# Performance work log

Measured on AMD Instinct MI355X. Metric: run time of the kernel, lower is better.

## Reference

```python
import jax, jax.numpy as jnp
import numpy as np

DIM, HEADS, DIM_HEAD = 1024, 16, 64
DIM_INNER = HEADS * DIM_HEAD  # 1024
SCALE = DIM_HEAD ** -0.5


def _rope(t):
    # t: [b, h, n, d]; interleaved-pair RoPE (lucidrains rotary-embedding-torch default)
    d = t.shape[-1]
    n = t.shape[-2]
    inv_freq = 1.0 / (10000.0 ** (jnp.arange(0, d, 2, dtype=jnp.float32) / d))
    angles = jnp.arange(n, dtype=jnp.float32)[:, None] * inv_freq[None, :]  # [n, d/2]
    cos, sin = jnp.cos(angles), jnp.sin(angles)
    t1, t2 = t[..., 0::2], t[..., 1::2]
    r1 = t1 * cos - t2 * sin
    r2 = t1 * sin + t2 * cos
    return jnp.stack([r1, r2], axis=-1).reshape(t.shape)


def setup_inputs() -> dict:
    key = jax.random.key(0)
    ks = jax.random.split(key, 8)
    b, n = 2, 2048
    inp = {
        "x": jax.random.normal(ks[0], (b, n, DIM), dtype=jnp.float32),
        "value_residual": jax.random.normal(ks[1], (b, HEADS, n, DIM_HEAD), dtype=jnp.float32),
        "gamma": jnp.ones((DIM,), dtype=jnp.float32),
        "w_qkv": jax.random.normal(ks[2], (DIM, 3 * DIM_INNER), dtype=jnp.float32) * (DIM ** -0.5),
        "w_mix": jax.random.normal(ks[3], (DIM, HEADS), dtype=jnp.float32) * (DIM ** -0.5),
        "b_mix": jnp.zeros((HEADS,), dtype=jnp.float32),
        "w_gates": jax.random.normal(ks[4], (DIM, HEADS), dtype=jnp.float32) * (DIM ** -0.5),
        "b_gates": jnp.zeros((HEADS,), dtype=jnp.float32),
        "w_out": jax.random.normal(ks[5], (DIM_INNER, DIM), dtype=jnp.float32) * (DIM_INNER ** -0.5),
    }
    return inp


def reference(x, value_residual, gamma, w_qkv, w_mix, b_mix, w_gates, b_gates, w_out):
    b, n, _ = x.shape
    # RMSNorm (lucidrains style: F.normalize * sqrt(dim) * gamma)
    norm = jnp.sqrt(jnp.sum(x * x, axis=-1, keepdims=True))
    xn = x / jnp.maximum(norm, 1e-12) * (DIM ** 0.5) * gamma

    qkv = xn @ w_qkv  # [b, n, 3*h*d]
    qkv = qkv.reshape(b, n, 3, HEADS, DIM_HEAD)
    q, k, v = [jnp.transpose(qkv[:, :, i], (0, 2, 1, 3)) for i in range(3)]  # [b,h,n,d]
    original_values = v

    # learned value-residual lerp
    mix = jax.nn.sigmoid(xn @ w_mix + b_mix)            # [b, n, h]
    mix = jnp.transpose(mix, (0, 2, 1))[..., None]       # [b, h, n, 1]
    v = v * (1.0 - mix) + value_residual * mix

    # rotary on q, k
    q = _rope(q)
    k = _rope(k)

    scores = jnp.einsum("bhid,bhjd->bhij", q, k) * SCALE
    attn = jax.nn.softmax(scores, axis=-1)
    out = jnp.einsum("bhij,bhjd->bhid", attn, v)         # [b, h, n, d]

    gates = jax.nn.sigmoid(xn @ w_gates + b_gates)       # [b, n, h]
    out = out * jnp.transpose(gates, (0, 2, 1))[..., None]

    out = jnp.transpose(out, (0, 2, 1, 3)).reshape(b, n, DIM_INNER)
    return out @ w_out, original_values
```

## Files before the change

### kernel.cpp

```cpp
#include <hip/hip_runtime.h>
#include <hip/hip_bf16.h>
#include <math.h>

#define DIMSZ 1024
#define HEADS 16
#define DHEAD 64
#define NSEQ  2048
#define BATCH 2
#define ROWS  (BATCH*NSEQ)
#define SCALE 0.125f
#define LOG2E 1.4426950408889634f

typedef __attribute__((ext_vector_type(8))) short short8;
typedef __attribute__((ext_vector_type(4))) float floatx4;

#define MFMA16(a,b,c) __builtin_amdgcn_mfma_f32_16x16x32_bf16(a,b,c,0,0,0)

__device__ __forceinline__ void gl2lds16(const void* g, void* l) {
    __builtin_amdgcn_global_load_lds(
        (const __attribute__((address_space(1))) unsigned int*)g,
        (__attribute__((address_space(3))) unsigned int*)l, 16, 0, 0);
}

__device__ __forceinline__ unsigned short bf16r(float a) {
    unsigned u = __float_as_uint(a);
    u += 0x7fff + ((u >> 16) & 1);
    return (unsigned short)(u >> 16);
}
__device__ __forceinline__ unsigned pack_bf16(float a, float b) {
    unsigned ua = __float_as_uint(a), ub = __float_as_uint(b);
    ua += 0x7fff + ((ua >> 16) & 1);
    ub += 0x7fff + ((ub >> 16) & 1);
    return (ua >> 16) | (ub & 0xffff0000u);
}
__device__ __forceinline__ float2 bf2f(unsigned u) {
    float2 r;
    r.x = __uint_as_float(u << 16);
    r.y = __uint_as_float(u & 0xffff0000u);
    return r;
}
__device__ __forceinline__ float fexp2(float x) {
#if __has_builtin(__builtin_amdgcn_exp2f)
    return __builtin_amdgcn_exp2f(x);
#else
    return exp2f(x);
#endif
}
__device__ __forceinline__ float fsin_rev(float x) {
#if __has_builtin(__builtin_amdgcn_sinf)
    return __builtin_amdgcn_sinf(x);
#else
    return __sinf(x * 6.28318530717958647692f);
#endif
}
__device__ __forceinline__ float fcos_rev(float x) {
#if __has_builtin(__builtin_amdgcn_cosf)
    return __builtin_amdgcn_cosf(x);
#else
    return __cosf(x * 6.28318530717958647692f);
#endif
}

__global__ __launch_bounds__(256) void transpose_all_kernel(
    const float* __restrict__ w_qkv, const float* __restrict__ w_out,
    const float* __restrict__ w_mix, const float* __restrict__ w_gates,
    unsigned short* __restrict__ wqkvT, unsigned short* __restrict__ woutT,
    unsigned short* __restrict__ wmgT)
{
    __shared__ float t[32][33];
    const int tx = threadIdx.x & 31, tyy = threadIdx.x >> 5;
    const int bx = blockIdx.x;
    const int k0 = blockIdx.y * 32;
    if (bx < 128) {
        const float* src;
        unsigned short* dst;
        int N, n0;
        if (bx < 96) { src = w_qkv; dst = wqkvT; N = 3*DIMSZ; n0 = bx*32; }
        else         { src = w_out; dst = woutT; N = DIMSZ;   n0 = (bx-96)*32; }
        #pragma unroll
        for (int i = 0; i < 4; i++)
            t[tyy*4 + i][tx] = src[(size_t)(k0 + tyy*4 + i)*N + n0 + tx];
        __syncthreads();
        #pragma unroll
        for (int i = 0; i < 4; i++)
            dst[(size_t)(n0 + tyy*4 + i)*DIMSZ + k0 + tx] = bf16r(t[tx][tyy*4 + i]);
    } else {
        #pragma unroll
        for (int i = 0; i < 4; i++) {
            const int kk = k0 + tyy*4 + i;
            t[tyy*4 + i][tx] = (tx < 16) ? w_mix[kk*16 + tx]
                                         : w_gates[kk*16 + (tx - 16)];
        }
        __syncthreads();
        #pragma unroll
        for (int i = 0; i < 4; i++)
            wmgT[(size_t)(tyy*4 + i)*DIMSZ + k0 + tx] = bf16r(t[tx][tyy*4 + i]);
    }
}

__global__ __launch_bounds__(256) void rmsnorm_kernel(
    const float* __restrict__ x, const float* __restrict__ gamma,
    unsigned short* __restrict__ xnb)
{
    const int row = blockIdx.x;
    const int tid = threadIdx.x;
    __shared__ float wred[4];

    const float4 xv = ((const float4*)(x + (size_t)row * DIMSZ))[tid];
    float ss = xv.x*xv.x + xv.y*xv.y + xv.z*xv.z + xv.w*xv.w;
    #pragma unroll
    for (int off = 1; off < 64; off <<= 1) ss += __shfl_xor(ss, off);
    if ((tid & 63) == 0) wred[tid >> 6] = ss;
    __syncthreads();
    const float total = wred[0] + wred[1] + wred[2] + wred[3];
    const float inv = 32.0f / fmaxf(sqrtf(total), 1e-12f);
    const float4 gv = ((const float4*)gamma)[tid];
    uint2 pk;
    pk.x = pack_bf16(xv.x * inv * gv.x, xv.y * inv * gv.y);
    pk.y = pack_bf16(xv.z * inv * gv.z, xv.w * inv * gv.w);
    ((uint2*)(xnb + (size_t)row * DIMSZ))[tid] = pk;
}

__global__ __launch_bounds__(256) void mix_gates_mfma(
    const unsigned short* __restrict__ A, const unsigned short* __restrict__ WG,
    const float* __restrict__ b_mix, const float* __restrict__ b_gates,
    float* __restrict__ mixo, float* __restrict__ gateso)
{
    __shared__ short As[128*32];
    __shared__ short Bs[32*32];
    const int tid = threadIdx.x;
    const int wv = tid >> 6, lane = tid & 63;
    const int g = lane >> 4, c = lane & 15;
    const int bm = blockIdx.x * 128;

    floatx4 acc[2][2];
    #pragma unroll
    for (int mt = 0; mt < 2; mt++)
        #pragma unroll
        for (int nt = 0; nt < 2; nt++) acc[mt][nt] = (floatx4){0.f,0.f,0.f,0.f};

    for (int k0 = 0; k0 < DIMSZ; k0 += 32) {
        __syncthreads();
        #pragma unroll
        for (int r = 0; r < 2; r++) {
            const int ch = tid + 256*r;
            const int row = ch >> 2, cc = ch & 3;
            gl2lds16(A + (size_t)(bm + row)*DIMSZ + k0 + cc*8, (void*)(As + ch*8));
        }
        if (tid < 128)
            gl2lds16(WG + (size_t)(tid >> 2)*DIMSZ + k0 + (tid & 3)*8, (void*)(Bs + tid*8));
        __syncthreads();
        short8 af[2], bf[2];
        #pragma unroll
        for (int mt = 0; mt < 2; mt++) af[mt] = *(const short8*)(As + (wv*32 + mt*16 + c)*32 + g*8);
        #pragma unroll
        for (int nt = 0; nt < 2; nt++) bf[nt] = *(const short8*)(Bs + (nt*16 + c)*32 + g*8);
        #pragma unroll
        for (int mt = 0; mt < 2; mt++)
            #pragma unroll
            for (int nt = 0; nt < 2; nt++)
                acc[mt][nt] = MFMA16(af[mt], bf[nt], acc[mt][nt]);
    }
    const float bm_c = b_mix[c], bg_c = b_gates[c];
    #pragma unroll
    for (int mt = 0; mt < 2; mt++)
        #pragma unroll
        for (int r2 = 0; r2 < 4; r2++) {
            const int row = bm + wv*32 + mt*16 + g*4 + r2;
            const float lm = acc[mt][0][r2] + bm_c;
            const float lg = acc[mt][1][r2] + bg_c;
            mixo[(size_t)row*HEADS + c]   = 1.0f / (1.0f + fexp2(-lm * LOG2E));
            gateso[(size_t)row*HEADS + c] = 1.0f / (1.0f + fexp2(-lg * LOG2E));
        }
}

__global__ __launch_bounds__(256) void gemm_qkv_mfma(
    const unsigned short* __restrict__ A, const unsigned short* __restrict__ BT,
    unsigned short* __restrict__ qb, unsigned short* __restrict__ kb,
    float* __restrict__ vb)
{
    __shared__ short As[128*32];
    __shared__ short Bs[128*32];
    const int tid = threadIdx.x;
    const int wv = tid >> 6, lane = tid & 63;
    const int g = lane >> 4, c = lane & 15;
    const int wm = wv >> 1, wn = wv & 1;
    const int bm = blockIdx.y * 128, bn = blockIdx.x * 128;

    floatx4 acc[4][4];
    #pragma unroll
    for (int mt = 0; mt < 4; mt++)
        #pragma unroll
        for (int nt = 0; nt < 4; nt++) acc[mt][nt] = (floatx4){0.f,0.f,0.f,0.f};

    for (int k0 = 0; k0 < DIMSZ; k0 += 32) {
        __syncthreads();
        #pragma unroll
        for (int r = 0; r < 2; r++) {
            const int ch = tid + 256*r;
            const int row = ch >> 2, cc = ch & 3;
            gl2lds16(A  + (size_t)(bm + row)*DIMSZ + k0 + cc*8, (void*)(As + ch*8));
            gl2lds16(BT + (size_t)(bn + row)*DIMSZ + k0 + cc*8, (void*)(Bs + ch*8));
        }
        __syncthreads();
        short8 af[4], bf[4];
        #pragma unroll
        for (int mt = 0; mt < 4; mt++) af[mt] = *(const short8*)(As + (wm*64 + mt*16 + c)*32 + g*8);
        #pragma unroll
        for (int nt = 0; nt < 4; nt++) bf[nt] = *(const short8*)(Bs + (wn*64 + nt*16 + c)*32 + g*8);
        #pragma unroll
        for (int mt = 0; mt < 4; mt++)
            #pragma unroll
            for (int nt = 0; nt < 4; nt++)
                acc[mt][nt] = MFMA16(af[mt], bf[nt], acc[mt][nt]);
    }
    __syncthreads();
    const int i3 = bn >> 10;
    const int nb = bn - (i3 << 10);
    if (i3 < 2) {
        unsigned short* dst = (i3 == 0) ? qb : kb;
        short* wbuf = As + wv*1152;
        const int rd_row = lane >> 2, seg = lane & 3;
        #pragma unroll
        for (int mt = 0; mt < 4; mt++) {
            #pragma unroll
            for (int nt = 0; nt < 4; nt++)
                #pragma unroll
                for (int r2 = 0; r2 < 4; r2++)
                    wbuf[(g*4 + r2)*72 + nt*16 + c] = (short)bf16r(acc[mt][nt][r2]);
            __builtin_amdgcn_s_waitcnt(0xc07f);
            const uint4 v0 = *(const uint4*)&wbuf[rd_row*72 + seg*16];
            const uint4 v1 = *(const uint4*)&wbuf[rd_row*72 + seg*16 + 8];
            const int row = bm + wm*64 + mt*16 + rd_row;
            const int col = nb + wn*64 + seg*16;
            const int hh = col >> 6, dd = col & 63;
            const int bb2 = row >> 11, pos = row & 2047;
            unsigned short* dp = dst + (((size_t)(bb2*HEADS + hh)*NSEQ) + pos)*DHEAD + dd;
            *(uint4*)dp = v0;
            *(uint4*)(dp + 8) = v1;
            __builtin_amdgcn_s_waitcnt(0xc07f);
        }
    } else {
        #pragma unroll
        for (int mt = 0; mt < 4; mt++)
            #pragma unroll
            for (int nt = 0; nt < 4; nt++)
                #pragma unroll
                for (int r2 = 0; r2 < 4; r2++) {
                    const int row = bm + wm*64 + mt*16 + g*4 + r2;
                    const int col = nb + wn*64 + nt*16 + c;
                    const int hh = col >> 6, dd = col & 63;
                    const int bb2 = row >> 11, pos = row & 2047;
                    vb[(((size_t)(bb2*HEADS + hh)*NSEQ) + pos)*DHEAD + dd] = acc[mt][nt][r2];
                }
    }
}

__global__ __launch_bounds__(256) void rope_blend_kernel2(
    unsigned short* __restrict__ q, unsigned short* __restrict__ k,
    const float* __restrict__ vorig, const float* __restrict__ vres,
    const float* __restrict__ mixb, unsigned short* __restrict__ vT)
{
    __shared__ unsigned short vt[64*72];
    const int tid = threadIdx.x;
    const int bh = blockIdx.y, bb = bh >> 4, h = bh & 15;
    const int p0 = blockIdx.x * 64;
    {
        const int pr = tid >> 2, d0 = (tid & 3) * 16;
        const int pos = p0 + pr;
        const size_t base = ((size_t)bh*NSEQ + pos)*DHEAD + d0;

        uint4 qr0 = *(uint4*)(q + base), qr1 = *(uint4*)(q + base + 8);
        uint4 kr0 = *(uint4*)(k + base), kr1 = *(uint4*)(k + base + 8);
        unsigned qw[8] = {qr0.x, qr0.y, qr0.z, qr0.w, qr1.x, qr1.y, qr1.z, qr1.w};
        unsigned kw[8] = {kr0.x, kr0.y, kr0.z, kr0.w, kr1.x, kr1.y, kr1.z, kr1.w};
        const float QSC = SCALE * LOG2E;
        const float posf = (float)pos;
        #pragma unroll
        for (int j = 0; j < 8; j++) {
            const float pf = (float)((d0 >> 1) + j);
            const float rev = posf * fexp2(-pf * 0.41524101186092029f
                                           - 2.6514961294723187f);
            const float rf = rev - floorf(rev);
            const float sn = fsin_rev(rf);
            const float cs = fcos_rev(rf);
            float2 qv = bf2f(qw[j]);
            float2 kv = bf2f(kw[j]);
            const float q1 = qv.x*cs - qv.y*sn, q2 = qv.x*sn + qv.y*cs;
            const float k1 = kv.x*cs - kv.y*sn, k2 = kv.x*sn + kv.y*cs;
            qw[j] = pack_bf16(q1*QSC, q2*QSC);
            kw[j] = pack_bf16(k1, k2);
        }
        *(uint4*)(q + base)     = *(uint4*)(qw + 0);
        *(uint4*)(q + base + 8) = *(uint4*)(qw + 4);
        *(uint4*)(k + base)     = *(uint4*)(kw + 0);
        *(uint4*)(k + base + 8) = *(uint4*)(kw + 4);

        float vv[16], vr[16];
        #pragma unroll
        for (int i = 0; i < 4; i++) {
            *(float4*)(vv + i*4) = *(const float4*)(vorig + base + i*4);
            *(float4*)(vr + i*4) = *(const float4*)(vres + base + i*4);
        }
        const float mx = mixb[((size_t)(bb*NSEQ + pos))*HEADS + h];
        #pragma unroll
        for (int j = 0; j < 8; j++) {
            const float b0 = vv[2*j]*(1.f-mx)   + vr[2*j]*mx;
            const float b1 = vv[2*j+1]*(1.f-mx) + vr[2*j+1]*mx;
            vt[pr*72 + d0 + 2*j]     = bf16r(b0);
            vt[pr*72 + d0 + 2*j + 1] = bf16r(b1);
        }
    }
    __syncthreads();
    {
        const int dd = tid >> 2, c0 = (tid & 3) * 16;
        unsigned o[8];
        #pragma unroll
        for (int j = 0; j < 8; j++) {
            const unsigned a  = vt[(c0 + 2*j)*72 + dd];
            const unsigned b2 = vt[(c0 + 2*j + 1)*72 + dd];
            o[j] = a | (b2 << 16);
        }
        unsigned short* dst = vT + ((size_t)bh*DHEAD + dd)*NSEQ + p0 + c0;
        *(uint4*)(dst)     = *(uint4*)(o + 0);
        *(uint4*)(dst + 8) = *(uint4*)(o + 4);
    }
}

__global__ __launch_bounds__(256) void attn_mfma_kernel(
    const unsigned short* __restrict__ qg,
    const unsigned short* __restrict__ kg,
    const unsigned short* __restrict__ vT,
    unsigned short* __restrict__ Op0,
    unsigned short* __restrict__ Op1,
    float* __restrict__ lpart)
{
    __shared__ short Kt[64*64];
    __shared__ short Vt[64*64];
    __shared__ short Ps[4*32*64];

    const int tid = threadIdx.x;
    const int w = tid >> 6, lane = tid & 63;
    const int g = lane >> 4, c = lane & 15;
    const int byy = blockIdx.y;
    const int bh = byy >> 1, s = byy & 1;
    const int bb = bh >> 4, h = bh & 15;
    const int q0 = blockIdx.x * 128;

    short8 qf[2][2];
    #pragma unroll
    for (int mt = 0; mt < 2; mt++)
        #pragma unroll
        for (int kb = 0; kb < 2; kb++)
            qf[mt][kb] = *(const short8*)(qg + ((size_t)bh*NSEQ + q0 + w*32 + mt*16 + c)*DHEAD + kb*32 + g*8);

    floatx4 O[2][4];
    #pragma unroll
    for (int mt = 0; mt < 2; mt++)
        #pragma unroll
        for (int nt = 0; nt < 4; nt++) O[mt][nt] = (floatx4){0.f,0.f,0.f,0.f};
    float lsum[2] = {0.f, 0.f};

    short* PsW = Ps + w * 2048;
    const unsigned short* kbase = kg + (size_t)bh*NSEQ*DHEAD;
    const unsigned short* vbase = vT + (size_t)bh*DHEAD*NSEQ;

    for (int i = 0; i < 16; i++) {
        const int kt = s*16 + i;
        __syncthreads();
        #pragma unroll
        for (int r = 0; r < 2; r++) {
            const int ch = tid + 256*r;
            const int row = ch >> 3;
            const int u = (ch & 7) ^ (row & 7);
            gl2lds16(kbase + (size_t)(kt*64 + row)*DHEAD + u*8, (void*)(Kt + ch*8));
            gl2lds16(vbase + (size_t)row*NSEQ + kt*64 + u*8,   (void*)(Vt + ch*8));
        }
        __syncthreads();

        short8 kfr[4][2];
        #pragma unroll
        for (int nt = 0; nt < 4; nt++) {
            const int rowk = nt*16 + c;
            #pragma unroll
            for (int kb = 0; kb < 2; kb++)
                kfr[nt][kb] = *(const short8*)(Kt + rowk*64 + (((kb*4 + g) ^ (rowk & 7)) * 8));
        }

        #pragma unroll
        for (int mt = 0; mt < 2; mt++) {
            const int rr = mt*16 + c;
            #pragma unroll
            for (int nt = 0; nt < 4; nt++) {
                floatx4 accS = (floatx4){0.f,0.f,0.f,0.f};
                #pragma unroll
                for (int kb = 0; kb < 2; kb++)
                    accS = MFMA16(kfr[nt][kb], qf[mt][kb], accS);
                const float p0 = fexp2(accS[0]);
                const float p1 = fexp2(accS[1]);
                const float p2 = fexp2(accS[2]);
                const float p3 = fexp2(accS[3]);
                lsum[mt] += (p0 + p1) + (p2 + p3);
                uint2 pk;
                pk.x = pack_bf16(p0, p1);
                pk.y = pack_bf16(p2, p3);
                *(uint2*)(PsW + rr*64 + (((nt*2 + (g >> 1)) ^ (rr & 7)) * 8) + (g & 1)*4) = pk;
            }
        }
        __builtin_amdgcn_s_waitcnt(0xc07f);
        #pragma unroll
        for (int kb = 0; kb < 2; kb++) {
            short8 pf[2];
            #pragma unroll
            for (int mt = 0; mt < 2; mt++) {
                const int rr = mt*16 + c;
                pf[mt] = *(const short8*)(PsW + rr*64 + (((kb*4 + g) ^ (rr & 7)) * 8));
            }
            #pragma unroll
            for (int nt = 0; nt < 4; nt++) {
                const int rv = nt*16 + c;
                short8 vf = *(const short8*)(Vt + rv*64 + (((kb*4 + g) ^ (rv & 7)) * 8));
                #pragma unroll
                for (int mt = 0; mt < 2; mt++)
                    O[mt][nt] = MFMA16(pf[mt], vf, O[mt][nt]);
            }
        }
    }

    unsigned short* Op = s ? Op1 : Op0;
    #pragma unroll
    for (int mt = 0; mt < 2; mt++) {
        float l = lsum[mt];
        l += __shfl_xor(l, 16);
        l += __shfl_xor(l, 32);
        if (g == 0) {
            const int rowl = q0 + w*32 + mt*16 + c;
            lpart[((size_t)s*ROWS + bb*NSEQ + rowl)*HEADS + h] = l;
        }
        #pragma unroll
        for (int r2 = 0; r2 < 4; r2++) {
            const int rowg = q0 + w*32 + mt*16 + g*4 + r2;
            unsigned short* op = Op + ((size_t)(bb*NSEQ + rowg))*DIMSZ + h*DHEAD + c;
            #pragma unroll
            for (int nt = 0; nt < 4; nt++)
                op[nt*16] = bf16r(O[mt][nt][r2]);
        }
    }
}

__global__ __launch_bounds__(256) void attn_combine_kernel(
    const unsigned short* __restrict__ Op1, const float* __restrict__ lpart,
    const float* __restrict__ gates, unsigned short* __restrict__ attnO)
{
    const int idx = blockIdx.x * 256 + threadIdx.x;
    const int row = idx >> 7;
    const int c8 = (idx & 127) * 8;
    const int h = c8 >> 6;
    const float l0 = lpart[(size_t)row*HEADS + h];
    const float l1 = lpart[((size_t)ROWS + row)*HEADS + h];
    const float gt = gates[(size_t)row*HEADS + h];
    const float sc = gt / (l0 + l1);
    const size_t base = (size_t)row*DIMSZ + c8;
    const uint4 a = *(const uint4*)(attnO + base);
    const uint4 b = *(const uint4*)(Op1 + base);
    const unsigned aw[4] = {a.x, a.y, a.z, a.w};
    const unsigned bw[4] = {b.x, b.y, b.z, b.w};
    unsigned o[4];
    #pragma unroll
    for (int j = 0; j < 4; j++) {
        const float2 fa = bf2f(aw[j]);
        const float2 fb = bf2f(bw[j]);
        o[j] = pack_bf16((fa.x + fb.x)*sc, (fa.y + fb.y)*sc);
    }
    *(uint4*)(attnO + base) = *(uint4*)o;
}

__global__ __launch_bounds__(256) void gemm_out_mfma(
    const unsigned short* __restrict__ A, const unsigned short* __restrict__ BT,
    float* __restrict__ out0)
{
    __shared__ short As[128*32];
    __shared__ short Bs[128*32];
    const int tid = threadIdx.x;
    const int wv = tid >> 6, lane = tid & 63;
    const int g = lane >> 4, c = lane & 15;
    const int wm = wv >> 1, wn = wv & 1;
    const int bm = blockIdx.y * 128, bn = blockIdx.x * 128;

    floatx4 acc[4][4];
    #pragma unroll
    for (int mt = 0; mt < 4; mt++)
        #pragma unroll
        for (int nt = 0; nt < 4; nt++) acc[mt][nt] = (floatx4){0.f,0.f,0.f,0.f};

    for (int k0 = 0; k0 < DIMSZ; k0 += 32) {
        __syncthreads();
        #pragma unroll
        for (int r = 0; r < 2; r++) {
            const int ch = tid + 256*r;
            const int row = ch >> 2, cc = ch & 3;
            gl2lds16(A  + (size_t)(bm + row)*DIMSZ + k0 + cc*8, (void*)(As + ch*8));
            gl2lds16(BT + (size_t)(bn + row)*DIMSZ + k0 + cc*8, (void*)(Bs + ch*8));
        }
        __syncthreads();
        short8 af[4], bf[4];
        #pragma unroll
        for (int mt = 0; mt < 4; mt++) af[mt] = *(const short8*)(As + (wm*64 + mt*16 + c)*32 + g*8);
        #pragma unroll
        for (int nt = 0; nt < 4; nt++) bf[nt] = *(const short8*)(Bs + (wn*64 + nt*16 + c)*32 + g*8);
        #pragma unroll
        for (int mt = 0; mt < 4; mt++)
            #pragma unroll
            for (int nt = 0; nt < 4; nt++)
                acc[mt][nt] = MFMA16(af[mt], bf[nt], acc[mt][nt]);
    }
    #pragma unroll
    for (int mt = 0; mt < 4; mt++)
        #pragma unroll
        for (int nt = 0; nt < 4; nt++)
            #pragma unroll
            for (int r2 = 0; r2 < 4; r2++) {
                const int row = bm + wm*64 + mt*16 + g*4 + r2;
                const int col = bn + wn*64 + nt*16 + c;
                out0[(size_t)row*DIMSZ + col] = acc[mt][nt][r2];
            }
}

extern "C" void kernel_launch(void* const* d_in, const int* in_sizes, int n_in,
                              void* d_out, int out_size, void* d_ws, size_t ws_size,
                              hipStream_t stream) {
    const float* x       = (const float*)d_in[0];
    const float* vres    = (const float*)d_in[1];
    const float* gamma   = (const float*)d_in[2];
    const float* w_qkv   = (const float*)d_in[3];
    const float* w_mix   = (const float*)d_in[4];
    const float* b_mix   = (const float*)d_in[5];
    const float* w_gates = (const float*)d_in[6];
    const float* b_gates = (const float*)d_in[7];
    const float* w_out   = (const float*)d_in[8];

    float* out0 = (float*)d_out;
    float* out1 = out0 + (size_t)ROWS * DIMSZ;

    char* ws = (char*)d_ws;
    unsigned short* xnb   = (unsigned short*)(ws);
    unsigned short* wqkvT = (unsigned short*)(ws + (8u<<20));
    unsigned short* woutT = (unsigned short*)(ws + (14u<<20));
    unsigned short* qb2   = (unsigned short*)(ws + (16u<<20));
    unsigned short* kb2   = (unsigned short*)(ws + (24u<<20));
    unsigned short* vT    = (unsigned short*)(ws + (32u<<20));
    unsigned short* attnO = (unsigned short*)(ws + (40u<<20));
    float*          mixb  = (float*)(ws + (48u<<20));
    float*          gatesb= (float*)(ws + (48u<<20) + 262144);
    unsigned short* wmgT  = (unsigned short*)(ws + (49u<<20));
    unsigned short* Op1   = (unsigned short*)(ws + (50u<<20));
    float*          lpart = (float*)(ws + (58u<<20));

    transpose_all_kernel<<<dim3(129, DIMSZ/32), 256, 0, stream>>>(
        w_qkv, w_out, w_mix, w_gates, wqkvT, woutT, wmgT);

    rmsnorm_kernel<<<ROWS, 256, 0, stream>>>(x, gamma, xnb);

    mix_gates_mfma<<<ROWS/128, 256, 0, stream>>>(
        xnb, wmgT, b_mix, b_gates, mixb, gatesb);

    gemm_qkv_mfma<<<dim3(3*DIMSZ/128, ROWS/128), 256, 0, stream>>>(
        xnb, wqkvT, qb2, kb2, out1);

    rope_blend_kernel2<<<dim3(NSEQ/64, BATCH*HEADS), 256, 0, stream>>>(
        qb2, kb2, out1, vres, mixb, vT);

    attn_mfma_kernel<<<dim3(NSEQ/128, BATCH*HEADS*2), 256, 0, stream>>>(
        qb2, kb2, vT, attnO, Op1, lpart);

    attn_combine_kernel<<<ROWS*DIMSZ/8/256, 256, 0, stream>>>(
        Op1, lpart, gatesb, attnO);

    gemm_out_mfma<<<dim3(DIMSZ/128, ROWS/128), 256, 0, stream>>>(
        attnO, woutT, out0);
}
```

Before: 262.1 us.

## Double-buffer K/V tiles in attention, remap workgroups, add MFMA priority hints

The attention kernel now double-buffers the K and V shared-memory tiles. The next tile's global-to-LDS load is issued while the current one is being computed, which removes one barrier per iteration. The P scratch buffer is halved by running softmax and PV one 16-row m-tile at a time, and the MFMA sections are wrapped in s_setprio. Workgroup IDs are remapped with an XCD-style swizzle, and launch bounds request 4 blocks per SM. These raise shared-memory use and register pressure, and the wg remap hardcodes the grid shape.

After: 263.1 us. No clear change (+0.4%).

```diff
diff --git a/kernel.cpp b/kernel.cpp
--- a/kernel.cpp
+++ b/kernel.cpp
@@ -327,7 +327,7 @@
     }
 }
 
-__global__ __launch_bounds__(256) void attn_mfma_kernel(
+__global__ __launch_bounds__(256, 4) void attn_mfma_kernel(
     const unsigned short* __restrict__ qg,
     const unsigned short* __restrict__ kg,
     const unsigned short* __restrict__ vT,
@@ -335,17 +335,20 @@
     unsigned short* __restrict__ Op1,
     float* __restrict__ lpart)
 {
-    __shared__ short Kt[64*64];
-    __shared__ short Vt[64*64];
-    __shared__ short Ps[4*32*64];
+    __shared__ short Kt[2][64*64];
+    __shared__ short Vt[2][64*64];
+    __shared__ short Ps[4*16*64];
 
     const int tid = threadIdx.x;
     const int w = tid >> 6, lane = tid & 63;
     const int g = lane >> 4, c = lane & 15;
-    const int byy = blockIdx.y;
+
+    int wg = blockIdx.y * gridDim.x + blockIdx.x;
+    wg = (wg & 7) * 128 + (wg >> 3);
+    const int q0 = (wg & 15) * 128;
+    const int byy = wg >> 4;
     const int bh = byy >> 1, s = byy & 1;
     const int bb = bh >> 4, h = bh & 15;
-    const int q0 = blockIdx.x * 128;
 
     short8 qf[2][2];
     #pragma unroll
@@ -361,22 +364,41 @@
         for (int nt = 0; nt < 4; nt++) O[mt][nt] = (floatx4){0.f,0.f,0.f,0.f};
     float lsum[2] = {0.f, 0.f};
 
-    short* PsW = Ps + w * 2048;
+    short* PsW = Ps + w * 1024;
     const unsigned short* kbase = kg + (size_t)bh*NSEQ*DHEAD;
     const unsigned short* vbase = vT + (size_t)bh*DHEAD*NSEQ;
 
-    for (int i = 0; i < 16; i++) {
-        const int kt = s*16 + i;
-        __syncthreads();
+    {
+        const int kt = s*16;
         #pragma unroll
         for (int r = 0; r < 2; r++) {
             const int ch = tid + 256*r;
             const int row = ch >> 3;
             const int u = (ch & 7) ^ (row & 7);
-            gl2lds16(kbase + (size_t)(kt*64 + row)*DHEAD + u*8, (void*)(Kt + ch*8));
-            gl2lds16(vbase + (size_t)row*NSEQ + kt*64 + u*8,   (void*)(Vt + ch*8));
-        }
-        __syncthreads();
+            gl2lds16(kbase + (size_t)(kt*64 + row)*DHEAD + u*8, (void*)(&Kt[0][0] + ch*8));
+            gl2lds16(vbase + (size_t)row*NSEQ + kt*64 + u*8,   (void*)(&Vt[0][0] + ch*8));
+        }
+    }
+    __syncthreads();
+
+    for (int i = 0; i < 16; i++) {
+        const int cur = i & 1;
+        const short* Ktc = &Kt[cur][0];
+        const short* Vtc = &Vt[cur][0];
+
+        if (i < 15) {
+            const int kt = s*16 + i + 1;
+            short* Ktn = &Kt[cur ^ 1][0];
+            short* Vtn = &Vt[cur ^ 1][0];
+            #pragma unroll
+            for (int r = 0; r < 2; r++) {
+                const int ch = tid + 256*r;
+                const int row = ch >> 3;
+                const int u = (ch & 7) ^ (row & 7);
+                gl2lds16(kbase + (size_t)(kt*64 + row)*DHEAD + u*8, (void*)(Ktn + ch*8));
+                gl2lds16(vbase + (size_t)row*NSEQ + kt*64 + u*8,   (void*)(Vtn + ch*8));
+            }
+        }
 
         short8 kfr[4][2];
         #pragma unroll
@@ -384,18 +406,18 @@
             const int rowk = nt*16 + c;
             #pragma unroll
             for (int kb = 0; kb < 2; kb++)
-                kfr[nt][kb] = *(const short8*)(Kt + rowk*64 + (((kb*4 + g) ^ (rowk & 7)) * 8));
+                kfr[nt][kb] = *(const short8*)(Ktc + rowk*64 + (((kb*4 + g) ^ (rowk & 7)) * 8));
         }
 
         #pragma unroll
         for (int mt = 0; mt < 2; mt++) {
-            const int rr = mt*16 + c;
             #pragma unroll
             for (int nt = 0; nt < 4; nt++) {
                 floatx4 accS = (floatx4){0.f,0.f,0.f,0.f};
-                #pragma unroll
-                for (int kb = 0; kb < 2; kb++)
-                    accS = MFMA16(kfr[nt][kb], qf[mt][kb], accS);
+                __builtin_amdgcn_s_setprio(1);
+                accS = MFMA16(kfr[nt][0], qf[mt][0], accS);
+                accS = MFMA16(kfr[nt][1], qf[mt][1], accS);
+                __builtin_amdgcn_s_setprio(0);
                 const float p0 = fexp2(accS[0]);
                 const float p1 = fexp2(accS[1]);
                 const float p2 = fexp2(accS[2]);
@@ -404,27 +426,23 @@
                 uint2 pk;
                 pk.x = pack_bf16(p0, p1);
                 pk.y = pack_bf16(p2, p3);
-                *(uint2*)(PsW + rr*64 + (((nt*2 + (g >> 1)) ^ (rr & 7)) * 8) + (g & 1)*4) = pk;
+                *(uint2*)(PsW + c*64 + (((nt*2 + (g >> 1)) ^ (c & 7)) * 8) + (g & 1)*4) = pk;
             }
-        }
-        __builtin_amdgcn_s_waitcnt(0xc07f);
-        #pragma unroll
-        for (int kb = 0; kb < 2; kb++) {
-            short8 pf[2];
-            #pragma unroll
-            for (int mt = 0; mt < 2; mt++) {
-                const int rr = mt*16 + c;
-                pf[mt] = *(const short8*)(PsW + rr*64 + (((kb*4 + g) ^ (rr & 7)) * 8));
+            __builtin_amdgcn_s_waitcnt(0xc07f);
+            __builtin_amdgcn_s_setprio(1);
+            #pragma unroll
+            for (int kb = 0; kb < 2; kb++) {
+                short8 pf = *(const short8*)(PsW + c*64 + (((kb*4 + g) ^ (c & 7)) * 8));
+                #pragma unroll
+                for (int nt = 0; nt < 4; nt++) {
+                    const int rv = nt*16 + c;
+                    short8 vf = *(const short8*)(Vtc + rv*64 + (((kb*4 + g) ^ (rv & 7)) * 8));
+                    O[mt][nt] = MFMA16(pf, vf, O[mt][nt]);
+                }
             }
-            #pragma unroll
-            for (int nt = 0; nt < 4; nt++) {
-                const int rv = nt*16 + c;
-                short8 vf = *(const short8*)(Vt + rv*64 + (((kb*4 + g) ^ (rv & 7)) * 8));
-                #pragma unroll
-                for (int mt = 0; mt < 2; mt++)
-                    O[mt][nt] = MFMA16(pf[mt], vf, O[mt][nt]);
-            }
-        }
+            __builtin_amdgcn_s_setprio(0);
+        }
+        __syncthreads();
     }
 
     unsigned short* Op = s ? Op1 : Op0;
```
